# Kernel tuning notes

Hardware: AMD Instinct MI355X
Metric: run time of the kernel (lower is better)

## Reference

```python
import jax, jax.numpy as jnp
import numpy as np

BANDS = [[0,63],[48,111],[96,159],[144,207],[192,255],[240,303],[288,351],[336,399],[384,447],[432,495],[480,543],[528,591],[576,639],[624,687],[672,735],[720,783],[768,831],[816,879],[864,927],[912,975],[960,1023],[961,1024]]
N_FFT, WIN, HOP, FREQ = 2048, 2048, 512, 1025
B, T, D = 8, 2048, 128
NB = len(BANDS)
WIDTH = BANDS[0][1] - BANDS[0][0] + 1  # 64, all bands equal width
STARTS = np.array([s for s, _ in BANDS])
POS = STARTS[:, None] + np.arange(WIDTH)[None, :]  # (NB, WIDTH) freq-bin indices


def setup_inputs() -> dict:
    key = jax.random.key(0)
    k1, k2, k3 = jax.random.split(key, 3)
    z = jax.random.normal(k1, (B, T, NB, D), jnp.float32)
    mix_spec = jax.random.normal(k2, (B, 2, T, FREQ), jnp.float32)
    W = jax.random.normal(k3, (NB, D, WIDTH * 2), jnp.float32) * 1e-4  # init std=0.0001
    b = jnp.zeros((NB, WIDTH * 2), jnp.float32).at[:, 0::2].set(1.0)   # real part bias = 1
    return {"z": z, "mix_spec": mix_spec, "W": W, "b": b}


def _istft(spec_r, spec_i):
    # spec_r/spec_i: (B, T, F) -> waveform (B, HOP*(T-1)), center=True semantics
    comp = spec_r + 1j * spec_i
    frames = jnp.fft.irfft(comp, n=N_FFT, axis=-1)  # (B, T, n_fft)
    n = jnp.arange(WIN, dtype=frames.dtype)
    win = 0.5 * (1.0 - jnp.cos(2.0 * jnp.pi * n / WIN))  # periodic Hann
    frames = frames * win
    total = HOP * (T - 1) + N_FFT
    pos = HOP * jnp.arange(T)[:, None] + jnp.arange(N_FFT)[None, :]  # (T, n_fft)
    out = jnp.zeros((frames.shape[0], total), frames.dtype).at[:, pos].add(frames)
    env = jnp.zeros((total,), frames.dtype).at[pos].add(win * win)
    out = out / jnp.where(env > 1e-11, env, 1.0)
    start = N_FFT // 2
    return out[:, start:start + HOP * (T - 1)]


def reference(z, mix_spec, W, b):
    # per-band linear projections (all same width -> one batched einsum)
    band = jnp.einsum('btnd,ndo->btno', z, W) + b          # (B, T, NB, 2*WIDTH)
    band = band.reshape(B, T, NB, WIDTH, 2)
    # scatter-add into overlapping frequency ranges + overlap-count normalization
    mask = jnp.zeros((B, T, FREQ, 2), z.dtype).at[:, :, POS, :].add(band)
    wgt = jnp.zeros((FREQ,), z.dtype).at[POS].add(1.0)
    mask = mask / jnp.maximum(wgt, 1.0)[None, None, :, None]
    mask_r, mask_i = mask[..., 0], mask[..., 1]            # (B, T, F)
    mix_r, mix_i = mix_spec[:, 0], mix_spec[:, 1]          # (B, T, F)
    out_r = mask_r * mix_r - mask_i * mix_i
    out_i = mask_r * mix_i + mask_i * mix_r
    return _istft(out_r, out_i)
```

## Files before the change

### kernel.cpp

```cpp
#include <hip/hip_runtime.h>

typedef _Float16 f16x8 __attribute__((ext_vector_type(8)));
typedef _Float16 f16x2 __attribute__((ext_vector_type(2)));
typedef float f32x4 __attribute__((ext_vector_type(4)));

#define SLOT_DW 2048
#define WT_BYTE_OFF 134217728
#define PHYS(i) ((i) + ((i) >> 5))

__device__ __forceinline__ void async_copy16(const void* g, void* l) {
  __builtin_amdgcn_global_load_lds((const __attribute__((address_space(1))) void*)g,
                                   (__attribute__((address_space(3))) void*)l, 16, 0, 0);
}

__global__ __launch_bounds__(256) void k_init(const float* __restrict__ W,
                                              _Float16* __restrict__ Wt) {
  int n = blockIdx.x >> 2, dq = blockIdx.x & 3;
  int tid = threadIdx.x;
  __shared__ _Float16 L[32 * 130];
  const float* Wn = W + (size_t)n * 16384 + dq * 32 * 128;
  for (int el = tid; el < 4096; el += 256) {
    int dl = el >> 7, o = el & 127;
    L[dl * 130 + o] = (_Float16)(Wn[el] * 4096.0f);
  }
  __syncthreads();
  _Float16* Wtn = Wt + (size_t)n * 16384 + dq * 32;
  for (int el = tid; el < 4096; el += 256) {
    int o = el >> 5, dl = el & 31;
    Wtn[o * 128 + dl] = L[dl * 130 + o];
  }
}

__global__ __launch_bounds__(256) void kA(const float* __restrict__ z,
                                          const _Float16* __restrict__ Wt,
                                          _Float16* __restrict__ band) {
  int mt = blockIdx.x;
  int n  = blockIdx.y;
  int r0 = mt * 64;
  __shared__ __align__(16) char smem[33280];
  int tid = threadIdx.x;
  int lane = tid & 63, wave = tid >> 6;
  int l16 = lane & 15, quad = lane >> 4;

  const _Float16* Wn = Wt + (size_t)n * 16384;
  f16x8 bfrag[8];
#pragma unroll
  for (int kb = 0; kb < 4; kb++) {
    int ko = kb * 32 + quad * 8;
    bfrag[2 * kb]     = *(const f16x8*)(Wn + (wave * 32 + l16) * 128 + ko);
    bfrag[2 * kb + 1] = *(const f16x8*)(Wn + (wave * 32 + 16 + l16) * 128 + ko);
  }

  {
    int col16 = lane & 31;
    int rowh  = lane >> 5;
#pragma unroll
    for (int it = 0; it < 8; it++) {
      int pr = wave * 8 + it;
      const float* g = z + ((size_t)(r0 + 2 * pr + rowh) * 22 + n) * 128 + col16 * 4;
      async_copy16(g, smem + pr * 1040);
    }
  }
  __syncthreads();

  f32x4 acc[2][4];
#pragma unroll
  for (int c = 0; c < 2; c++)
#pragma unroll
    for (int rt = 0; rt < 4; rt++) acc[c][rt] = (f32x4){0.f, 0.f, 0.f, 0.f};

#pragma unroll
  for (int kb = 0; kb < 4; kb++) {
#pragma unroll
    for (int rt = 0; rt < 4; rt++) {
      int row = rt * 16 + l16;
      const float* ap = (const float*)(smem + (row >> 1) * 1040 + (row & 1) * 512) + kb * 32 + quad * 8;
      float4 v0 = *(const float4*)ap;
      float4 v1 = *(const float4*)(ap + 4);
      f16x8 a;
      a[0] = (_Float16)v0.x; a[1] = (_Float16)v0.y; a[2] = (_Float16)v0.z; a[3] = (_Float16)v0.w;
      a[4] = (_Float16)v1.x; a[5] = (_Float16)v1.y; a[6] = (_Float16)v1.z; a[7] = (_Float16)v1.w;
      acc[0][rt] = __builtin_amdgcn_mfma_f32_16x16x32_f16(a, bfrag[2 * kb],     acc[0][rt], 0, 0, 0);
      acc[1][rt] = __builtin_amdgcn_mfma_f32_16x16x32_f16(a, bfrag[2 * kb + 1], acc[1][rt], 0, 0, 0);
    }
  }
  __syncthreads();

  _Float16* Cs = (_Float16*)smem;
  const float inv_scale = 1.0f / 4096.0f;
#pragma unroll
  for (int c = 0; c < 2; c++) {
    int col = (wave * 2 + c) * 16 + l16;
#pragma unroll
    for (int rt = 0; rt < 4; rt++) {
#pragma unroll
      for (int reg = 0; reg < 4; reg++) {
        int row = rt * 16 + quad * 4 + reg;
        Cs[row * 136 + col] = (_Float16)(acc[c][rt][reg] * inv_scale);
      }
    }
  }
  __syncthreads();
  int row = tid >> 2;
  int c4 = (tid & 3) * 32;
  const _Float16* srcl = &Cs[row * 136 + c4];
  _Float16* dst = band + (size_t)(r0 + row) * (SLOT_DW * 2) + n * 128 + c4;
  f16x8 v0 = *(const f16x8*)(srcl);
  f16x8 v1 = *(const f16x8*)(srcl + 8);
  f16x8 v2 = *(const f16x8*)(srcl + 16);
  f16x8 v3 = *(const f16x8*)(srcl + 24);
  *(f16x8*)(dst)      = v0;
  *(f16x8*)(dst + 8)  = v1;
  *(f16x8*)(dst + 16) = v2;
  *(f16x8*)(dst + 24) = v3;
}

__global__ __launch_bounds__(256) void kB(const float* __restrict__ mix,
                                          const float* __restrict__ bias,
                                          float* __restrict__ ws) {
  int r = blockIdx.x;
  int b = r >> 11, t = r & 2047;
  __shared__ __align__(16) float2 bufA[1056];
  __shared__ __align__(16) float2 bufB[1056];
  int tid = threadIdx.x;

  const _Float16* bandg = (const _Float16*)(ws + (size_t)r * SLOT_DW);
  const float2* bias2 = (const float2*)bias;
  const float* mixr = mix + ((size_t)(b * 2) * 2048 + t) * 1025;
  const float* mixi = mix + ((size_t)(b * 2 + 1) * 2048 + t) * 1025;

  for (int k = tid; k <= 512; k += 256) {
    float2 X[2];
#pragma unroll
    for (int side = 0; side < 2; side++) {
      int f = side ? (1024 - k) : k;
      float mr = 0.f, mi = 0.f;
      int wgt = 0;
      int nhi = f / 48; if (nhi > 20) nhi = 20;
      int nlo = (f >= 16) ? (f - 16) / 48 : 0;
      for (int n = nlo; n <= nhi; n++) {
        int idx = n * 128 + 2 * (f - n * 48);
        f16x2 bv = *(const f16x2*)(bandg + idx);
        float2 bb = bias2[idx >> 1];
        mr += (float)bv[0] + bb.x;
        mi += (float)bv[1] + bb.y;
        wgt++;
      }
      if (f >= 961) {
        int idx = 21 * 128 + 2 * (f - 961);
        f16x2 bv = *(const f16x2*)(bandg + idx);
        float2 bb = bias2[idx >> 1];
        mr += (float)bv[0] + bb.x;
        mi += (float)bv[1] + bb.y;
        wgt++;
      }
      float inv = (wgt == 1) ? 1.0f : ((wgt == 2) ? 0.5f : (1.0f / 3.0f));
      mr *= inv; mi *= inv;
      float xr = mixr[f], xi = mixi[f];
      float outr = mr * xr - mi * xi;
      float outi = mr * xi + mi * xr;
      if (f == 0 || f == 1024) outi = 0.0f;
      X[side] = make_float2(outr, outi);
      if (k == 512) { X[1] = X[0]; break; }
    }
    float Ar = X[0].x + X[1].x, Ai = X[0].y - X[1].y;
    float Br = X[0].x - X[1].x, Bi = X[0].y + X[1].y;
    float sv, cv;
    __sincosf((float)k * 3.0679615757712823e-3f, &sv, &cv);
    float s1 = cv * Bi + sv * Br;
    float s2 = cv * Br - sv * Bi;
    bufA[PHYS(k & 1023)] = make_float2(Ar - s1, Ai + s2);
    if (k > 0 && k < 512) bufA[PHYS(1024 - k)] = make_float2(Ar + s1, -Ai + s2);
  }

  float2* src = bufA;
  float2* dst = bufB;
#pragma unroll
  for (int st = 0; st < 5; st++) {
    const int s = 2 * st;
    const int m = 1 << s;
    __syncthreads();
    int q = tid >> s, rr = tid & (m - 1);
    float2 x0 = src[PHYS(tid)];
    float2 x1 = src[PHYS(tid + 256)];
    float2 x2 = src[PHYS(tid + 512)];
    float2 x3 = src[PHYS(tid + 768)];
    float ang = (float)(q * m) * 6.135923151542565e-3f;
    float ws1, wc1;
    __sincosf(ang, &ws1, &wc1);
    float wc2 = wc1 * wc1 - ws1 * ws1, ws2 = 2.0f * wc1 * ws1;
    float wc3 = wc2 * wc1 - ws2 * ws1, ws3 = wc2 * ws1 + ws2 * wc1;
    float tAr = x0.x + x2.x, tAi = x0.y + x2.y;
    float tBr = x0.x - x2.x, tBi = x0.y - x2.y;
    float tCr = x1.x + x3.x, tCi = x1.y + x3.y;
    float tDr = x1.x - x3.x, tDi = x1.y - x3.y;
    int base = 4 * q * m + rr;
    dst[PHYS(base)] = make_float2(tAr + tCr, tAi + tCi);
    float pr = tBr - tDi, pi = tBi + tDr;
    dst[PHYS(base + m)] = make_float2(wc1 * pr - ws1 * pi, wc1 * pi + ws1 * pr);
    float qr = tAr - tCr, qi = tAi - tCi;
    dst[PHYS(base + 2 * m)] = make_float2(wc2 * qr - ws2 * qi, wc2 * qi + ws2 * qr);
    float rr2 = tBr + tDi, ri2 = tBi - tDr;
    dst[PHYS(base + 3 * m)] = make_float2(wc3 * rr2 - ws3 * ri2, wc3 * ri2 + ws3 * rr2);
    float2* tmp = src; src = dst; dst = tmp;
  }
  __syncthreads();

  float2* slot2 = (float2*)(ws + (size_t)r * SLOT_DW);
  const float inv_n = 1.0f / 2048.0f;
  for (int j = tid; j < 1024; j += 256) {
    float2 g = src[PHYS(j)];
    float c0 = __cosf((float)(2 * j) * 3.0679615757712823e-3f);
    float c1 = __cosf((float)(2 * j + 1) * 3.0679615757712823e-3f);
    float w0 = 0.5f * (1.0f - c0);
    float w1 = 0.5f * (1.0f - c1);
    slot2[j] = make_float2(g.x * inv_n * w0, g.y * inv_n * w1);
  }
}

__global__ __launch_bounds__(256) void kC(const float* __restrict__ ws,
                                          float* __restrict__ out) {
  int b = blockIdx.y;
  int p = blockIdx.x * 256 + threadIdx.x;
  int q = p + 1024;
  int t0 = (q - 1536) >> 9; if (t0 < 0) t0 = 0;
  int t1 = q >> 9;          if (t1 > 2047) t1 = 2047;
  float sum = 0.f;
  for (int t = t0; t <= t1; t++) {
    int i = q - (t << 9);
    sum += ws[(size_t)(b * 2048 + t) * SLOT_DW + i];
  }
  float env;
  if (t1 - t0 == 3) {
    env = 1.5f;
  } else {
    env = 0.f;
    for (int t = t0; t <= t1; t++) {
      int i = q - (t << 9);
      float c = __cosf((float)i * 3.0679615757712823e-3f);
      float win = 0.5f * (1.0f - c);
      env += win * win;
    }
  }
  out[(size_t)b * 1048064 + p] = sum / (env > 1e-11f ? env : 1.0f);
}

extern "C" void kernel_launch(void* const* d_in, const int* in_sizes, int n_in,
                              void* d_out, int out_size, void* d_ws, size_t ws_size,
                              hipStream_t stream) {
  const float* z    = (const float*)d_in[0];
  const float* mix  = (const float*)d_in[1];
  const float* W    = (const float*)d_in[2];
  const float* bias = (const float*)d_in[3];
  float* out = (float*)d_out;
  _Float16* Wt = (_Float16*)((char*)d_ws + WT_BYTE_OFF);

  k_init<<<88, 256, 0, stream>>>(W, Wt);
  kA<<<dim3(256, 22), 256, 0, stream>>>(z, Wt, (_Float16*)d_ws);
  kB<<<16384, 256, 0, stream>>>(mix, bias, (float*)d_ws);
  kC<<<dim3(4094, 8), 256, 0, stream>>>((const float*)d_ws, out);
}
```

Baseline: 487.7 us.

## Loop kA over bands with double-buffered z loads; vectorize kC overlap-add

kA now gives each block 16 rows and loops over all 22 bands. It double-buffers the async z loads into LDS so the next band's fetch overlaps the current MFMA and store, and it reloads W fragments for each band. kC now handles four output samples per thread using float4 loads of the frame slots, with a scalar fallback near frame boundaries. The aim is to cut launch and block count and to raise memory-access width, at the cost of more barriers per block and smaller MFMA tiles in kA.

```diff
diff --git a/kernel.cpp b/kernel.cpp
--- a/kernel.cpp
+++ b/kernel.cpp
@@ -34,85 +34,68 @@
 __global__ __launch_bounds__(256) void kA(const float* __restrict__ z,
                                           const _Float16* __restrict__ Wt,
                                           _Float16* __restrict__ band) {
-  int mt = blockIdx.x;
-  int n  = blockIdx.y;
-  int r0 = mt * 64;
-  __shared__ __align__(16) char smem[33280];
+  int r0 = blockIdx.x * 16;
+  __shared__ __align__(16) char bufZ[2][8 * 1040];
+  __shared__ __align__(16) _Float16 Cs[16 * 136];
   int tid = threadIdx.x;
   int lane = tid & 63, wave = tid >> 6;
   int l16 = lane & 15, quad = lane >> 4;
-
-  const _Float16* Wn = Wt + (size_t)n * 16384;
-  f16x8 bfrag[8];
-#pragma unroll
-  for (int kb = 0; kb < 4; kb++) {
-    int ko = kb * 32 + quad * 8;
-    bfrag[2 * kb]     = *(const f16x8*)(Wn + (wave * 32 + l16) * 128 + ko);
-    bfrag[2 * kb + 1] = *(const f16x8*)(Wn + (wave * 32 + 16 + l16) * 128 + ko);
-  }
-
+  int col16 = lane & 31, rowh = lane >> 5;
+
+  int pr0 = wave * 2;
   {
-    int col16 = lane & 31;
-    int rowh  = lane >> 5;
-#pragma unroll
-    for (int it = 0; it < 8; it++) {
-      int pr = wave * 8 + it;
-      const float* g = z + ((size_t)(r0 + 2 * pr + rowh) * 22 + n) * 128 + col16 * 4;
-      async_copy16(g, smem + pr * 1040);
-    }
-  }
-  __syncthreads();
-
-  f32x4 acc[2][4];
-#pragma unroll
-  for (int c = 0; c < 2; c++)
-#pragma unroll
-    for (int rt = 0; rt < 4; rt++) acc[c][rt] = (f32x4){0.f, 0.f, 0.f, 0.f};
-
-#pragma unroll
-  for (int kb = 0; kb < 4; kb++) {
-#pragma unroll
-    for (int rt = 0; rt < 4; rt++) {
-      int row = rt * 16 + l16;
-      const float* ap = (const float*)(smem + (row >> 1) * 1040 + (row & 1) * 512) + kb * 32 + quad * 8;
+    const float* g0 = z + ((size_t)(r0 + 2 * pr0 + rowh) * 22 + 0) * 128 + col16 * 4;
+    const float* g1 = z + ((size_t)(r0 + 2 * pr0 + 2 + rowh) * 22 + 0) * 128 + col16 * 4;
+    async_copy16(g0, &bufZ[0][pr0 * 1040]);
+    async_copy16(g1, &bufZ[0][(pr0 + 1) * 1040]);
+  }
+
+  for (int n = 0; n < 22; n++) {
+    __syncthreads();
+    int cur = n & 1;
+    const _Float16* Wn = Wt + (size_t)n * 16384;
+    f16x8 b0[4], b1[4];
+#pragma unroll
+    for (int kb = 0; kb < 4; kb++) {
+      int ko = kb * 32 + quad * 8;
+      b0[kb] = *(const f16x8*)(Wn + (wave * 32 + l16) * 128 + ko);
+      b1[kb] = *(const f16x8*)(Wn + (wave * 32 + 16 + l16) * 128 + ko);
+    }
+    f32x4 a0 = (f32x4){0.f, 0.f, 0.f, 0.f};
+    f32x4 a1 = (f32x4){0.f, 0.f, 0.f, 0.f};
+    const float* bz = (const float*)&bufZ[cur][0];
+    int abase = (l16 >> 1) * 260 + (l16 & 1) * 128 + quad * 8;
+#pragma unroll
+    for (int kb = 0; kb < 4; kb++) {
+      const float* ap = bz + abase + kb * 32;
       float4 v0 = *(const float4*)ap;
       float4 v1 = *(const float4*)(ap + 4);
       f16x8 a;
       a[0] = (_Float16)v0.x; a[1] = (_Float16)v0.y; a[2] = (_Float16)v0.z; a[3] = (_Float16)v0.w;
       a[4] = (_Float16)v1.x; a[5] = (_Float16)v1.y; a[6] = (_Float16)v1.z; a[7] = (_Float16)v1.w;
-      acc[0][rt] = __builtin_amdgcn_mfma_f32_16x16x32_f16(a, bfrag[2 * kb],     acc[0][rt], 0, 0, 0);
-      acc[1][rt] = __builtin_amdgcn_mfma_f32_16x16x32_f16(a, bfrag[2 * kb + 1], acc[1][rt], 0, 0, 0);
-    }
-  }
-  __syncthreads();
-
-  _Float16* Cs = (_Float16*)smem;
-  const float inv_scale = 1.0f / 4096.0f;
-#pragma unroll
-  for (int c = 0; c < 2; c++) {
-    int col = (wave * 2 + c) * 16 + l16;
-#pragma unroll
-    for (int rt = 0; rt < 4; rt++) {
-#pragma unroll
-      for (int reg = 0; reg < 4; reg++) {
-        int row = rt * 16 + quad * 4 + reg;
-        Cs[row * 136 + col] = (_Float16)(acc[c][rt][reg] * inv_scale);
-      }
-    }
-  }
-  __syncthreads();
-  int row = tid >> 2;
-  int c4 = (tid & 3) * 32;
-  const _Float16* srcl = &Cs[row * 136 + c4];
-  _Float16* dst = band + (size_t)(r0 + row) * (SLOT_DW * 2) + n * 128 + c4;
-  f16x8 v0 = *(const f16x8*)(srcl);
-  f16x8 v1 = *(const f16x8*)(srcl + 8);
-  f16x8 v2 = *(const f16x8*)(srcl + 16);
-  f16x8 v3 = *(const f16x8*)(srcl + 24);
-  *(f16x8*)(dst)      = v0;
-  *(f16x8*)(dst + 8)  = v1;
-  *(f16x8*)(dst + 16) = v2;
-  *(f16x8*)(dst + 24) = v3;
+      a0 = __builtin_amdgcn_mfma_f32_16x16x32_f16(a, b0[kb], a0, 0, 0, 0);
+      a1 = __builtin_amdgcn_mfma_f32_16x16x32_f16(a, b1[kb], a1, 0, 0, 0);
+    }
+    const float inv_scale = 1.0f / 4096.0f;
+#pragma unroll
+    for (int reg = 0; reg < 4; reg++) {
+      int row = quad * 4 + reg;
+      Cs[row * 136 + (wave * 2) * 16 + l16]     = (_Float16)(a0[reg] * inv_scale);
+      Cs[row * 136 + (wave * 2 + 1) * 16 + l16] = (_Float16)(a1[reg] * inv_scale);
+    }
+    __syncthreads();
+    {
+      int row = tid >> 4, c8 = (tid & 15) * 8;
+      f16x8 v = *(const f16x8*)&Cs[row * 136 + c8];
+      *(f16x8*)(band + (size_t)(r0 + row) * (SLOT_DW * 2) + n * 128 + c8) = v;
+    }
+    if (n + 1 < 22) {
+      const float* g0 = z + ((size_t)(r0 + 2 * pr0 + rowh) * 22 + (n + 1)) * 128 + col16 * 4;
+      const float* g1 = z + ((size_t)(r0 + 2 * pr0 + 2 + rowh) * 22 + (n + 1)) * 128 + col16 * 4;
+      async_copy16(g0, &bufZ[cur ^ 1][pr0 * 1040]);
+      async_copy16(g1, &bufZ[cur ^ 1][(pr0 + 1) * 1040]);
+    }
+  }
 }
 
 __global__ __launch_bounds__(256) void kB(const float* __restrict__ mix,
@@ -221,28 +204,57 @@
 __global__ __launch_bounds__(256) void kC(const float* __restrict__ ws,
                                           float* __restrict__ out) {
   int b = blockIdx.y;
-  int p = blockIdx.x * 256 + threadIdx.x;
-  int q = p + 1024;
-  int t0 = (q - 1536) >> 9; if (t0 < 0) t0 = 0;
-  int t1 = q >> 9;          if (t1 > 2047) t1 = 2047;
-  float sum = 0.f;
-  for (int t = t0; t <= t1; t++) {
-    int i = q - (t << 9);
-    sum += ws[(size_t)(b * 2048 + t) * SLOT_DW + i];
-  }
-  float env;
-  if (t1 - t0 == 3) {
-    env = 1.5f;
+  int p0 = (blockIdx.x * 256 + threadIdx.x) * 4;
+  if (p0 >= 1048064) return;
+  int q0 = p0 + 1024;
+  int tA = (q0 >= 1536) ? ((q0 - 1536) >> 9) : 0;
+  int tB = (q0 + 3) >> 9; if (tB > 2047) tB = 2047;
+  const float* base = ws + (size_t)b * 2048 * SLOT_DW;
+  float s0 = 0.f, s1 = 0.f, s2 = 0.f, s3 = 0.f;
+  if ((q0 & 511) <= 508) {
+    for (int t = tA; t <= tB; t++) {
+      int i0 = q0 - (t << 9);
+      float4 v = *(const float4*)(base + (size_t)t * SLOT_DW + i0);
+      s0 += v.x; s1 += v.y; s2 += v.z; s3 += v.w;
+    }
   } else {
-    env = 0.f;
-    for (int t = t0; t <= t1; t++) {
-      int i = q - (t << 9);
-      float c = __cosf((float)i * 3.0679615757712823e-3f);
-      float win = 0.5f * (1.0f - c);
-      env += win * win;
-    }
-  }
-  out[(size_t)b * 1048064 + p] = sum / (env > 1e-11f ? env : 1.0f);
+    for (int t = tA; t <= tB; t++) {
+      int i0 = q0 - (t << 9);
+      const float* fp = base + (size_t)t * SLOT_DW;
+#pragma unroll
+      for (int j = 0; j < 4; j++) {
+        int i = i0 + j;
+        float v = (i >= 0 && i < 2048) ? fp[i] : 0.f;
+        float* sp = (j == 0) ? &s0 : (j == 1) ? &s1 : (j == 2) ? &s2 : &s3;
+        *sp += v;
+      }
+    }
+  }
+  float4 r;
+  float* sv[4] = {&s0, &s1, &s2, &s3};
+  float rv[4];
+#pragma unroll
+  for (int j = 0; j < 4; j++) {
+    int q = q0 + j;
+    float env;
+    if (q >= 1536 && q <= 1048575) {
+      env = 1.5f;
+    } else {
+      env = 0.f;
+      int t0e = (q >= 1536) ? ((q - 1536) >> 9) : 0;
+      int t1e = q >> 9; if (t1e > 2047) t1e = 2047;
+      for (int t = t0e; t <= t1e; t++) {
+        int i = q - (t << 9);
+        float c = __cosf((float)i * 3.0679615757712823e-3f);
+        float win = 0.5f * (1.0f - c);
+        env += win * win;
+      }
+      if (env <= 1e-11f) env = 1.0f;
+    }
+    rv[j] = *sv[j] / env;
+  }
+  r.x = rv[0]; r.y = rv[1]; r.z = rv[2]; r.w = rv[3];
+  *(float4*)(out + (size_t)b * 1048064 + p0) = r;
 }
 
 extern "C" void kernel_launch(void* const* d_in, const int* in_sizes, int n_in,
@@ -256,7 +268,7 @@
   _Float16* Wt = (_Float16*)((char*)d_ws + WT_BYTE_OFF);
 
   k_init<<<88, 256, 0, stream>>>(W, Wt);
-  kA<<<dim3(256, 22), 256, 0, stream>>>(z, Wt, (_Float16*)d_ws);
+  kA<<<1024, 256, 0, stream>>>(z, Wt, (_Float16*)d_ws);
   kB<<<16384, 256, 0, stream>>>(mix, bias, (float*)d_ws);
-  kC<<<dim3(4094, 8), 256, 0, stream>>>((const float*)d_ws, out);
-}
+  kC<<<dim3(1024, 8), 256, 0, stream>>>((const float*)d_ws, out);
+}
```

New measurement: 504.0 us. 1.03x slower.
